# Optimization experiments

Hardware: AMD Instinct MI355X
Metric: run time of the kernel (lower is better)

Reference implementation:

```python
import jax, jax.numpy as jnp
import numpy as np

BS, GS, E, KMAX = 128, 2000, 128, 4
CLIP = 10.0
NEG = -1e30


def _gru(x, hprev, Wih, Whh, bih, bhh):
    # torch.nn.GRUCell math
    gi = x @ Wih.T + bih
    gh = hprev @ Whh.T + bhh
    ir, iz, i_n = jnp.split(gi, 3, axis=-1)
    hr, hz, h_n = jnp.split(gh, 3, axis=-1)
    r = jax.nn.sigmoid(ir + hr)
    z = jax.nn.sigmoid(iz + hz)
    n = jnp.tanh(i_n + r * h_n)
    return (1.0 - z) * n + z * hprev


def setup_inputs() -> dict:
    key = jax.random.key(0)
    it = iter(jax.random.split(key, 40))
    s = 1.0 / float(np.sqrt(E))
    u = lambda shape: jax.random.uniform(next(it), shape, jnp.float32, -s, s)
    inp = {
        "h": jax.random.normal(next(it), (BS, GS, E), jnp.float32),
        "rec": jax.random.randint(next(it), (BS, GS), 0, GS, dtype=jnp.int32),
        "context2": jax.random.normal(next(it), (BS, 9), jnp.float32),
        "visited_time": jax.random.randint(next(it), (BS, GS), 0, GS, dtype=jnp.int32),
        "last_action": jax.random.randint(next(it), (BS, 1), 0, GS, dtype=jnp.int32),
        "fixed_action": jax.random.randint(next(it), (BS, KMAX), 0, GS, dtype=jnp.int32),
    }
    for n in ["W_K1", "W_K2", "W_K3", "W_K4", "W_Q1", "W_Q2", "W_Q3", "W_Q4", "W_init"]:
        inp[n] = u((E, E))
    for n in ["b_init", "V1", "V2", "init_query"]:
        inp[n] = u((E,))
    for r in ["rnn1", "rnn2"]:
        inp[r + "_Wih"] = u((3 * E, E))
        inp[r + "_Whh"] = u((3 * E, E))
        inp[r + "_bih"] = u((3 * E,))
        inp[r + "_bhh"] = u((3 * E,))
    return inp


def _forward(h, rec, visited_time, last_action, fixed_action,
             W_K1, W_K2, W_K3, W_K4, W_Q1, W_Q2, W_Q3, W_Q4, V1, V2,
             W_init, b_init, init_query,
             rnn1_Wih, rnn1_Whh, rnn1_bih, rnn1_bhh,
             rnn2_Wih, rnn2_Whh, rnn2_bih, rnn2_bhh):
    bs, gs, e = h.shape
    cols = jnp.arange(gs)[None, :]          # [1, gs]
    rows = jnp.arange(bs)
    # K projections of h are loop-invariant: hoist them (same math as in-loop recompute)
    K1h = jnp.einsum('bge,fe->bgf', h, W_K1)
    K2h = jnp.einsum('bge,fe->bgf', h, W_K2)
    K3h = jnp.einsum('bge,fe->bgf', h, W_K3)
    K4h = jnp.einsum('bge,fe->bgf', h, W_K4)
    q1 = q2 = h.mean(1) @ W_init.T + b_init
    input_q1 = input_q2 = jnp.broadcast_to(init_query, (bs, e))
    mask = jnp.zeros((bs, gs), bool)
    stopped = jnp.ones((bs,), bool)
    nol = jnp.full((bs, 1), -1, jnp.int32)   # next_of_last_action
    ai = jnp.zeros((bs, KMAX), jnp.int32)    # action_index
    kl = jnp.zeros((bs, KMAX + 1), jnp.int32)
    kr = jnp.zeros((bs, KMAX), jnp.int32)
    ll = jnp.zeros((bs,), h.dtype)
    vtt = None
    for i in range(KMAX):
        q1 = _gru(input_q1, q1, rnn1_Wih, rnn1_Whh, rnn1_bih, rnn1_bhh)
        q2 = _gru(input_q2, q2, rnn2_Wih, rnn2_Whh, rnn2_bih, rnn2_bhh)
        s1 = (V1 * jnp.tanh(K1h + (q1 @ W_Q1.T)[:, None, :] + K3h * (q1 @ W_Q3.T)[:, None, :])).sum(-1)
        s2 = (V2 * jnp.tanh(K2h + (q2 @ W_Q2.T)[:, None, :] + K4h * (q2 @ W_Q4.T)[:, None, :])).sum(-1)
        logits = jnp.tanh(s1 + s2) * CLIP
        logits = jnp.where(mask, NEG, logits)
        if i == 0:
            logits = jnp.where(cols == last_action, NEG, logits)
        action = fixed_action[:, i:i + 1]
        if i > 0:
            action = jnp.where(stopped[:, None], ai[:, 0:1], action)
        logp = jax.nn.log_softmax(logits, axis=-1)
        loss_now = jnp.take_along_axis(logp, action, 1)[:, 0]
        ll = ll + (loss_now if i == 0 else jnp.where(stopped, 0.0, loss_now))
        nna = jnp.take_along_axis(rec, action, 1)  # next_of_new_action [bs,1]
        ai = ai.at[:, i].set(action[:, 0])
        kl = kl.at[:, i].set(jnp.where(stopped, action[:, 0], kl[:, i]))
        kr = kr.at[:, (i - 1) % KMAX].set(jnp.where(stopped, kr[:, (i - 1) % KMAX], action[:, 0]))
        kl = kl.at[:, i + 1].set(nna[:, 0])
        input_q1 = h[rows, action[:, 0]]
        input_q2 = jnp.where(stopped[:, None], input_q1, h[rows, nol[:, 0] % gs])
        eq = (action == nol)[:, 0]
        stopped = eq if i == 0 else (stopped | eq)
        kl = kl.at[:, i].set(jnp.where(stopped, kl[:, (i - 1) % (KMAX + 1)], kl[:, i]))
        kr = kr.at[:, i].set(jnp.where(stopped, kr[:, (i - 1) % KMAX], kr[:, i]))
        if i == 0:
            vtt = (visited_time - jnp.take_along_axis(visited_time, action, 1)) % gs
        vtt_a = jnp.take_along_axis(vtt, action, 1)
        mask = vtt <= vtt_a
        if i == 0:
            mask = mask | (vtt > gs - 2)
        mask = jnp.where(stopped[:, None] & (cols == action), False, mask)
        allow = (~stopped) & (nna[:, 0] == ai[:, 0])
        mask = jnp.where(allow[:, None] & (cols == ai[:, 0:1]), False, mask)
        nol = jnp.where(stopped[:, None], jnp.int32(-1), nna)
    kr = kr.at[:, KMAX - 1].set(jnp.where(~stopped, kl[:, KMAX], kr[:, KMAX - 1]))
    action_all = jnp.concatenate([ai, kl[:, :KMAX], kr], axis=-1)  # [bs, 3*KMAX]
    return action_all, ll


def reference(h, rec, context2, visited_time, last_action, fixed_action,
              W_K1, W_K2, W_K3, W_K4, W_Q1, W_Q2, W_Q3, W_Q4,
              V1, V2, W_init, b_init, init_query,
              rnn1_Wih, rnn1_Whh, rnn1_bih, rnn1_bhh,
              rnn2_Wih, rnn2_Whh, rnn2_bih, rnn2_bhh):
    # context2 unused: with_explore_stat_feature=False path (learned V1/V2)
    return _forward(h, rec, visited_time, last_action, fixed_action,
                    W_K1, W_K2, W_K3, W_K4, W_Q1, W_Q2, W_Q3, W_Q4, V1, V2,
                    W_init, b_init, init_query,
                    rnn1_Wih, rnn1_Whh, rnn1_bih, rnn1_bhh,
                    rnn2_Wih, rnn2_Whh, rnn2_bih, rnn2_bhh)
```

## Files before the change

### kernel.cpp

```cpp
#include <hip/hip_runtime.h>
#include <math.h>

#define BS 128
#define GS 2000
#define E  128
#define KMAXI 4
#define CLIPV 10.0f
#define NEGV  -1.0e30f

typedef __bf16 bf16_t;
typedef __bf16 bf16x8 __attribute__((ext_vector_type(8)));
typedef float fx4 __attribute__((ext_vector_type(4)));
typedef float fx2 __attribute__((ext_vector_type(2)));

__device__ __forceinline__ float fast_sigmoid(float x){ return 1.0f/(1.0f+__expf(-x)); }
__device__ __forceinline__ float fast_tanhf(float x){
    float e = __expf(2.0f*x);
    return 1.0f - 2.0f/(e + 1.0f);
}
__device__ __forceinline__ float pade_tanh(float x){
    float t = __builtin_amdgcn_fmed3f(x, -3.0f, 3.0f);
    float r = t*t;
    float num = t*(27.0f + r);
    float den = fmaf(9.0f, r, 27.0f);
    return num * __builtin_amdgcn_rcpf(den);
}
__device__ __forceinline__ fx2 tanh2_poly(fx2 x){
    fx2 t;
    t.x = __builtin_amdgcn_fmed3f(x.x, -3.0f, 3.0f);
    t.y = __builtin_amdgcn_fmed3f(x.y, -3.0f, 3.0f);
    fx2 r = t*t;
    fx2 q = r*(-0.0015650f) + 0.03172875f;
    q = q*r + (-0.23082094f);
    q = q*r + 0.979947f;
    return t*q;
}
__device__ __forceinline__ int pymod_s(int a){ return a < 0 ? a + GS : a; }

__device__ __forceinline__ void load_lds16(const bf16_t* g, bf16_t* l){
    __builtin_amdgcn_global_load_lds(
        (const __attribute__((address_space(1))) void*)g,
        (__attribute__((address_space(3))) void*)l, 16, 0, 0);
}

#define SC_STRIDE 64

__global__ __launch_bounds__(256) void k_hmean(
    const float* __restrict__ h, float* __restrict__ hpart,
    const int* __restrict__ rec, const int* __restrict__ vtime,
    const int* __restrict__ last_action, const int* __restrict__ fixed_action,
    int* __restrict__ sc, float* __restrict__ out)
{
    int b = blockIdx.x, p = blockIdx.y, tid = threadIdx.x;
    if (p == 16){
        if (b != 0) return;
        int t = tid;
        if (t >= BS) return;
        int stopped = 1, nol = -1;
        int ai[4]={0,0,0,0}, kl[5]={0,0,0,0,0}, kr[4]={0,0,0,0};
        int a0 = 0;
        int* scb = sc + t*SC_STRIDE;
        for (int it=0; it<KMAXI; ++it){
            int action = (it==0) ? fixed_action[t*KMAXI]
                                 : (stopped ? ai[0] : fixed_action[t*KMAXI+it]);
            int old_stopped = stopped;
            if (it==0) a0 = action;
            int vta = (it==0) ? 0 : pymod_s(vtime[(size_t)t*GS+action] - vtime[(size_t)t*GS+a0]);
            int nna = rec[(size_t)t*GS+action];
            int eq  = (action == nol) ? 1 : 0;
            int new_stopped = (it==0) ? eq : (stopped | eq);
            int ai0 = (it==0) ? action : ai[0];
            int allow = (!new_stopped) && (nna == ai0);

            ai[it] = action;
            if (old_stopped)  kl[it] = action;
            if (!old_stopped) kr[(it+3)&3] = action;
            kl[it+1] = nna;
            if (new_stopped) kl[it] = kl[(it+4)%5];
            if (new_stopped) kr[it] = kr[(it+3)&3];

            int row1 = action;
            int i2 = pymod_s(nol);
            int row2 = old_stopped ? row1 : i2;

            int* s_it = scb + 8 + it*8;
            s_it[0]=action; s_it[1]=old_stopped; s_it[2]=new_stopped;
            s_it[3]=allow;  s_it[4]=vta; s_it[5]=row1; s_it[6]=row2;

            nol = new_stopped ? -1 : nna;
            stopped = new_stopped;
        }
        scb[0] = a0;
        if (!stopped) kr[3] = kl[4];
        for (int j=0;j<4;++j) out[t*12+j]   = (float)ai[j];
        for (int j=0;j<4;++j) out[t*12+4+j] = (float)kl[j];
        for (int j=0;j<4;++j) out[t*12+8+j] = (float)kr[j];
        return;
    }
    int e4 = (tid & 31) * 4;
    int gsub = tid >> 5;
    float4 acc = {0.f,0.f,0.f,0.f};
    int g0 = p*125, g1 = g0+125;
    for (int g = g0 + gsub; g < g1; g += 8){
        float4 v = *(const float4*)(h + ((size_t)b*GS + g)*E + e4);
        acc.x += v.x; acc.y += v.y; acc.z += v.z; acc.w += v.w;
    }
    __shared__ float ps[8][E];
    *(float4*)(&ps[gsub][e4]) = acc;
    __syncthreads();
    if (tid < E){
        float s = 0.f;
        #pragma unroll
        for (int j=0;j<8;++j) s += ps[j][tid];
        hpart[(b*16+p)*E + tid] = s;
    }
}

__device__ __forceinline__ float dot32(const float* a, const float* __restrict__ w){
    const float4* a4=(const float4*)a; const float4* w4=(const float4*)w;
    float s=0.f;
    #pragma unroll 8
    for (int i=0;i<32;++i){ float4 x=a4[i], y=w4[i]; s += x.x*y.x + x.y*y.y + x.z*y.z + x.w*y.w; }
    return s;
}

__global__ __launch_bounds__(384) void k_gru4(
    const float* __restrict__ hpart, const float* __restrict__ W_init,
    const float* __restrict__ b_init, const float* __restrict__ init_query,
    const float* __restrict__ h, const int* __restrict__ sc,
    const float* __restrict__ Wih1, const float* __restrict__ Whh1,
    const float* __restrict__ bih1, const float* __restrict__ bhh1,
    const float* __restrict__ Wih2, const float* __restrict__ Whh2,
    const float* __restrict__ bih2, const float* __restrict__ bhh2,
    const float* __restrict__ WQ1, const float* __restrict__ WQ2,
    const float* __restrict__ WQ3, const float* __restrict__ WQ4,
    float* __restrict__ add_buf, float* __restrict__ mul_buf)
{
    int b = blockIdx.x, rnn = blockIdx.y, t = threadIdx.x;
    const float* Wih = rnn ? Wih2 : Wih1;
    const float* Whh = rnn ? Whh2 : Whh1;
    const float* bih = rnn ? bih2 : bih1;
    const float* bhh = rnn ? bhh2 : bhh1;
    const float* WQa = rnn ? WQ2 : WQ1;
    const float* WQm = rnn ? WQ4 : WQ3;

    __shared__ float xv[E], hv[E];
    __shared__ float gi_s[3*E], gh_s[3*E];

    if (t < E){
        float s = 0.f;
        for (int p=0;p<16;++p) s += hpart[(b*16+p)*E + t];
        xv[t] = s * (1.0f/(float)GS);
    }
    __syncthreads();
    if (t < E) hv[t] = b_init[t] + dot32(xv, W_init + (size_t)t*E);
    __syncthreads();
    if (t < E) xv[t] = init_query[t];
    __syncthreads();

    for (int s=0; s<KMAXI; ++s){
        if (s>0){
            if (t < E){
                int row = sc[b*SC_STRIDE + 8 + (s-1)*8 + (rnn==0 ? 5 : 6)];
                xv[t] = h[((size_t)b*GS + row)*E + t];
            }
            __syncthreads();
        }
        {
            float gi = bih[t] + dot32(xv, Wih + (size_t)t*E);
            float gh = bhh[t] + dot32(hv, Whh + (size_t)t*E);
            gi_s[t] = gi; gh_s[t] = gh;
        }
        __syncthreads();
        if (t < E){
            float r = fast_sigmoid(gi_s[t]     + gh_s[t]);
            float z = fast_sigmoid(gi_s[t+E]   + gh_s[t+E]);
            float n = fast_tanhf  (gi_s[t+2*E] + r*gh_s[t+2*E]);
            hv[t] = (1.f-z)*n + z*hv[t];
        }
        __syncthreads();
        if (t < 2*E){
            int r = t & (E-1);
            const float* W = (t < E) ? WQa : WQm;
            float v = dot32(hv, W + (size_t)r*E);
            int slot = s*2 + rnn;
            if (t < E) add_buf[(size_t)slot*BS*E + b*E + r] = v;
            else       mul_buf[(size_t)slot*BS*E + b*E + r] = v;
        }
        __syncthreads();
    }
}

__global__ __launch_bounds__(256) void k_mbuild(
    const float* __restrict__ WK1, const float* __restrict__ WK2,
    const float* __restrict__ WK3, const float* __restrict__ WK4,
    const float* __restrict__ mul_buf, bf16_t* __restrict__ Mb)
{
    int b = blockIdx.x, slot = blockIdx.y, tid = threadIdx.x;
    int arm = slot & 1;
    const float* WKa = arm ? WK2 : WK1;
    const float* WKm = arm ? WK4 : WK3;
    const float* mul = mul_buf + (size_t)slot*BS*E + b*E;
    __shared__ float mv[E];
    if (tid < E) mv[tid] = mul[tid];
    __syncthreads();
    bf16x8* outp = (bf16x8*)(Mb + ((size_t)slot*BS + b)*E*E);
    #pragma unroll
    for (int j=0;j<8;++j){
        int u = j*256 + tid;
        int f = u >> 4, e8 = u & 15;
        int e0 = e8*8;
        float mf = mv[f];
        float4 a0 = *(const float4*)(WKa + (size_t)f*E + e0);
        float4 a1 = *(const float4*)(WKa + (size_t)f*E + e0 + 4);
        float4 m0 = *(const float4*)(WKm + (size_t)f*E + e0);
        float4 m1 = *(const float4*)(WKm + (size_t)f*E + e0 + 4);
        bf16x8 o;
        o[0]=(bf16_t)(a0.x + m0.x*mf);
        o[1]=(bf16_t)(a0.y + m0.y*mf);
        o[2]=(bf16_t)(a0.z + m0.z*mf);
        o[3]=(bf16_t)(a0.w + m0.w*mf);
        o[4]=(bf16_t)(a1.x + m1.x*mf);
        o[5]=(bf16_t)(a1.y + m1.y*mf);
        o[6]=(bf16_t)(a1.z + m1.z*mf);
        o[7]=(bf16_t)(a1.w + m1.w*mf);
        outp[f*16 + (e8 ^ (f&7))] = o;
    }
}

__global__ __launch_bounds__(256,2) void k_scores(
    const float* __restrict__ hf, const bf16_t* __restrict__ Mb,
    const float* __restrict__ add_buf,
    const float* __restrict__ V1, const float* __restrict__ V2,
    const int* __restrict__ vtime, const int* __restrict__ last_action,
    const int* __restrict__ sc,
    float* __restrict__ part, float* __restrict__ act_val)
{
    __shared__ bf16_t sM[2][E*E];
    __shared__ float redm[16], reds[16];
    __shared__ float bmxs;
    int b = blockIdx.x, yc = blockIdx.y, tid = threadIdx.x;
    int wave = tid >> 6, lane = tid & 63;
    int qd = lane >> 4, cl = lane & 15;
    int gbase = yc*128 + wave*32;

    {
        const bf16_t* G0 = Mb + (size_t)b*E*E;
        #pragma unroll
        for (int j=0;j<8;++j){
            int c = wave*512 + j*64 + lane;
            load_lds16(G0 + (size_t)c*8, &sM[0][0] + (size_t)c*8);
        }
    }

    const int* scb = sc + b*SC_STRIDE;
    int a0s = scb[0];
    int la  = last_action[b];
    int vt0 = vtime[(size_t)b*GS + a0s];

    float vv_r[2][8];
    #pragma unroll
    for (int tf=0; tf<8; ++tf){
        vv_r[0][tf] = V1[tf*16+cl];
        vv_r[1][tf] = V2[tf*16+cl];
    }

    bf16x8 afr[2][4];
    #pragma unroll
    for (int set=0; set<2; ++set){
        int grow = gbase + set*16 + cl;
        if (grow >= GS) grow = GS-1;
        const float* hrow = hf + ((size_t)b*GS + grow)*E;
        #pragma unroll
        for (int s=0;s<4;++s){
            const float* p = hrow + s*32 + qd*8;
            float4 u0 = *(const float4*)(p);
            float4 u1 = *(const float4*)(p+4);
            bf16x8 a;
            a[0]=(bf16_t)u0.x; a[1]=(bf16_t)u0.y; a[2]=(bf16_t)u0.z; a[3]=(bf16_t)u0.w;
            a[4]=(bf16_t)u1.x; a[5]=(bf16_t)u1.y; a[6]=(bf16_t)u1.z; a[7]=(bf16_t)u1.w;
            afr[set][s]=a;
        }
    }
    __syncthreads();

    for (int it=0; it<KMAXI; ++it){
        fx2 s00={0.f,0.f}, s01={0.f,0.f}, s10={0.f,0.f}, s11={0.f,0.f};
        #pragma unroll
        for (int arm=0; arm<2; ++arm){
            int slot = it*2 + arm;
            int cur = slot & 1;
            if (slot < 7){
                const bf16_t* Gn = Mb + ((size_t)(slot+1)*BS + b)*E*E;
                #pragma unroll
                for (int j=0;j<8;++j){
                    int c = wave*512 + j*64 + lane;
                    load_lds16(Gn + (size_t)c*8, &sM[cur^1][0] + (size_t)c*8);
                }
            }
            const float* addv = add_buf + (size_t)slot*BS*E + b*E;
            float av_r[8];
            #pragma unroll
            for (int tf=0; tf<8; ++tf) av_r[tf] = addv[tf*16+cl];

            const bf16_t* sMc = &sM[cur][0];
            #pragma unroll
            for (int tf=0; tf<8; ++tf){
                int f = tf*16 + cl;
                bf16x8 b1[4];
                #pragma unroll
                for (int s=0;s<4;++s){
                    int e8 = s*4 + qd;
                    b1[s] = *(const bf16x8*)(sMc + ((size_t)(f*16 + (e8 ^ (f&7))))*8);
                }
                float av = av_r[tf];
                fx4 a0 = {av,av,av,av};
                fx4 a1 = {av,av,av,av};
                #pragma unroll
                for (int s=0;s<4;++s){
                    a0 = __builtin_amdgcn_mfma_f32_16x16x32_bf16(afr[0][s], b1[s], a0, 0,0,0);
                    a1 = __builtin_amdgcn_mfma_f32_16x16x32_bf16(afr[1][s], b1[s], a1, 0,0,0);
                }
                fx2 vv2 = {vv_r[arm][tf], vv_r[arm][tf]};
                s00 += vv2 * tanh2_poly((fx2){a0[0], a0[1]});
                s01 += vv2 * tanh2_poly((fx2){a0[2], a0[3]});
                s10 += vv2 * tanh2_poly((fx2){a1[0], a1[1]});
                s11 += vv2 * tanh2_poly((fx2){a1[2], a1[3]});
            }
            __syncthreads();
        }

        float vfin[2][4];
        #pragma unroll
        for (int set=0;set<2;++set){
            fx2 pa = set ? s10 : s00;
            fx2 pb = set ? s11 : s01;
            float v[4] = {pa.x, pa.y, pb.x, pb.y};
            #pragma unroll
            for (int r=0;r<4;++r){
                float s = v[r];
                s += __shfl_xor(s, 1); s += __shfl_xor(s, 2);
                s += __shfl_xor(s, 4); s += __shfl_xor(s, 8);
                vfin[set][r] = s;
            }
        }

        int act = scb[8 + it*8 + 0];
        int ap=0, nsp=0, alp=0, vtp=0;
        if (it>0){
            const int* s_p = scb + 8 + (it-1)*8;
            ap = s_p[0]; nsp = s_p[2]; alp = s_p[3]; vtp = s_p[4];
        }
        float x[8];
        float lm = NEGV;
        if (cl==0){
            #pragma unroll
            for (int set=0;set<2;++set){
                #pragma unroll
                for (int r=0;r<4;++r){
                    int idx = set*4 + r;
                    int g = gbase + set*16 + qd*4 + r;
                    float o = CLIPV*pade_tanh(vfin[set][r]);
                    int valid = (g < GS);
                    int gi = valid ? g : (GS-1);
                    int msk;
                    if (it==0){
                        msk = (g==la);
                    } else {
                        int d = vtime[(size_t)b*GS + gi] - vt0;
                        if (d < 0) d += GS;
                        msk = (d <= vtp) ? 1 : 0;
                        if (it==1 && d > GS-2) msk = 1;
                        if (nsp && g==ap)      msk = 0;
                        if (alp && g==a0s)     msk = 0;
                    }
                    float xx = (valid && !msk) ? o : NEGV;
                    if (valid && g==act) act_val[(size_t)it*BS + b] = xx;
                    x[idx] = xx;
                    lm = fmaxf(lm, xx);
                }
            }
            redm[wave*4+qd] = lm;
        }
        __syncthreads();
        if (tid==0){
            float m = redm[0];
            #pragma unroll
            for (int i=1;i<16;++i) m = fmaxf(m, redm[i]);
            bmxs = m;
        }
        __syncthreads();
        float bm = bmxs;
        if (cl==0){
            float ls = 0.f;
            #pragma unroll
            for (int i=0;i<8;++i) ls += __expf(x[i]-bm);
            reds[wave*4+qd] = ls;
        }
        __syncthreads();
        if (tid==0){
            float ss = 0.f;
            #pragma unroll
            for (int i=0;i<16;++i) ss += reds[i];
            fx2 pr = {bm, ss};
            *(fx2*)(part + (((size_t)it*BS + b)*16 + yc)*2) = pr;
        }
    }
}

__global__ __launch_bounds__(128) void k_final(
    const float* __restrict__ part, const float* __restrict__ act_val,
    const int* __restrict__ sc, float* __restrict__ out)
{
    int b = threadIdx.x;
    if (b >= BS) return;
    const int* scb = sc + b*SC_STRIDE;
    float ll = 0.f;
    for (int it=0; it<KMAXI; ++it){
        const fx2* pp = (const fx2*)(part + (((size_t)it*BS + b)*16)*2);
        float M = NEGV;
        #pragma unroll
        for (int i=0;i<16;++i) M = fmaxf(M, pp[i].x);
        float S = 0.f;
        #pragma unroll
        for (int i=0;i<16;++i) S += pp[i].y * __expf(pp[i].x - M);
        float lse = M + __logf(S);
        float av = act_val[(size_t)it*BS + b];
        int olds = scb[8 + it*8 + 1];
        if (it==0 || !olds) ll += av - lse;
    }
    out[BS*12 + b] = ll;
}

extern "C" void kernel_launch(void* const* d_in, const int* in_sizes, int n_in,
                              void* d_out, int out_size, void* d_ws, size_t ws_size,
                              hipStream_t stream)
{
    const float* h            = (const float*)d_in[0];
    const int*   rec          = (const int*)  d_in[1];
    const int*   vtime        = (const int*)  d_in[3];
    const int*   last_action  = (const int*)  d_in[4];
    const int*   fixed_action = (const int*)  d_in[5];
    const float* WK1=(const float*)d_in[6],  *WK2=(const float*)d_in[7];
    const float* WK3=(const float*)d_in[8],  *WK4=(const float*)d_in[9];
    const float* WQ1=(const float*)d_in[10], *WQ2=(const float*)d_in[11];
    const float* WQ3=(const float*)d_in[12], *WQ4=(const float*)d_in[13];
    const float* W_init=(const float*)d_in[14];
    const float* b_init=(const float*)d_in[15];
    const float* V1=(const float*)d_in[16], *V2=(const float*)d_in[17];
    const float* init_query=(const float*)d_in[18];
    const float* Wih1=(const float*)d_in[19], *Whh1=(const float*)d_in[20];
    const float* bih1=(const float*)d_in[21], *bhh1=(const float*)d_in[22];
    const float* Wih2=(const float*)d_in[23], *Whh2=(const float*)d_in[24];
    const float* bih2=(const float*)d_in[25], *bhh2=(const float*)d_in[26];
    float* out = (float*)d_out;

    char* ws = (char*)d_ws;
    size_t off = 0;
    auto alloc = [&](size_t bytes)->char*{
        char* p = ws + off; off += (bytes + 255) & ~(size_t)255; return p;
    };
    bf16_t* Mb     = (bf16_t*)alloc((size_t)8*BS*E*E*sizeof(bf16_t));
    float*  add_buf= (float*) alloc((size_t)8*BS*E*sizeof(float));
    float*  mul_buf= (float*) alloc((size_t)8*BS*E*sizeof(float));
    float*  hpart  = (float*) alloc((size_t)BS*16*E*sizeof(float));
    int*    sc     = (int*)   alloc((size_t)BS*SC_STRIDE*sizeof(int));
    float*  part   = (float*) alloc((size_t)KMAXI*BS*16*2*sizeof(float));
    float*  actv   = (float*) alloc((size_t)KMAXI*BS*sizeof(float));
    (void)in_sizes; (void)n_in; (void)out_size; (void)ws_size;

    hipLaunchKernelGGL(k_hmean, dim3(BS,17), dim3(256), 0, stream,
                       h, hpart, rec, vtime, last_action, fixed_action, sc, out);
    hipLaunchKernelGGL(k_gru4, dim3(BS,2), dim3(384), 0, stream,
                       hpart, W_init, b_init, init_query, h, sc,
                       Wih1,Whh1,bih1,bhh1, Wih2,Whh2,bih2,bhh2,
                       WQ1,WQ2,WQ3,WQ4, add_buf, mul_buf);
    hipLaunchKernelGGL(k_mbuild, dim3(BS,8), dim3(256), 0, stream,
                       WK1,WK2,WK3,WK4, mul_buf, Mb);
    hipLaunchKernelGGL(k_scores, dim3(BS,16), dim3(256), 0, stream,
                       h, Mb, add_buf, V1, V2, vtime, last_action, sc, part, actv);
    hipLaunchKernelGGL(k_final, dim3(1), dim3(128), 0, stream,
                       part, actv, sc, out);
}
```

Before: 460.5 us.

## Single-buffer M tile in LDS and move block softmax reduction to final kernel

```diff
diff --git a/kernel.cpp b/kernel.cpp
--- a/kernel.cpp
+++ b/kernel.cpp
@@ -236,22 +236,11 @@
     const int* __restrict__ sc,
     float* __restrict__ part, float* __restrict__ act_val)
 {
-    __shared__ bf16_t sM[2][E*E];
-    __shared__ float redm[16], reds[16];
-    __shared__ float bmxs;
+    __shared__ bf16_t sM[E*E];
     int b = blockIdx.x, yc = blockIdx.y, tid = threadIdx.x;
     int wave = tid >> 6, lane = tid & 63;
     int qd = lane >> 4, cl = lane & 15;
     int gbase = yc*128 + wave*32;
-
-    {
-        const bf16_t* G0 = Mb + (size_t)b*E*E;
-        #pragma unroll
-        for (int j=0;j<8;++j){
-            int c = wave*512 + j*64 + lane;
-            load_lds16(G0 + (size_t)c*8, &sM[0][0] + (size_t)c*8);
-        }
-    }
 
     const int* scb = sc + b*SC_STRIDE;
     int a0s = scb[0];
@@ -282,28 +271,27 @@
             afr[set][s]=a;
         }
     }
-    __syncthreads();
 
     for (int it=0; it<KMAXI; ++it){
         fx2 s00={0.f,0.f}, s01={0.f,0.f}, s10={0.f,0.f}, s11={0.f,0.f};
         #pragma unroll
         for (int arm=0; arm<2; ++arm){
             int slot = it*2 + arm;
-            int cur = slot & 1;
-            if (slot < 7){
-                const bf16_t* Gn = Mb + ((size_t)(slot+1)*BS + b)*E*E;
-                #pragma unroll
-                for (int j=0;j<8;++j){
-                    int c = wave*512 + j*64 + lane;
-                    load_lds16(Gn + (size_t)c*8, &sM[cur^1][0] + (size_t)c*8);
-                }
+            const bf16_t* Gm = Mb + ((size_t)slot*BS + b)*E*E;
+            const float* addv = add_buf + (size_t)slot*BS*E + b*E;
+
+            float av_r[8];
+            #pragma unroll
+            for (int tf=0; tf<8; ++tf) av_r[tf] = addv[tf*16+cl];
+
+            __syncthreads();
+            #pragma unroll
+            for (int j=0;j<8;++j){
+                int c = wave*512 + j*64 + lane;
+                load_lds16(Gm + (size_t)c*8, sM + (size_t)c*8);
             }
-            const float* addv = add_buf + (size_t)slot*BS*E + b*E;
-            float av_r[8];
-            #pragma unroll
-            for (int tf=0; tf<8; ++tf) av_r[tf] = addv[tf*16+cl];
-
-            const bf16_t* sMc = &sM[cur][0];
+            __syncthreads();
+
             #pragma unroll
             for (int tf=0; tf<8; ++tf){
                 int f = tf*16 + cl;
@@ -311,7 +299,7 @@
                 #pragma unroll
                 for (int s=0;s<4;++s){
                     int e8 = s*4 + qd;
-                    b1[s] = *(const bf16x8*)(sMc + ((size_t)(f*16 + (e8 ^ (f&7))))*8);
+                    b1[s] = *(const bf16x8*)(sM + ((size_t)(f*16 + (e8 ^ (f&7))))*8);
                 }
                 float av = av_r[tf];
                 fx4 a0 = {av,av,av,av};
@@ -327,7 +315,6 @@
                 s10 += vv2 * tanh2_poly((fx2){a1[0], a1[1]});
                 s11 += vv2 * tanh2_poly((fx2){a1[2], a1[3]});
             }
-            __syncthreads();
         }
 
         float vfin[2][4];
@@ -351,9 +338,9 @@
             const int* s_p = scb + 8 + (it-1)*8;
             ap = s_p[0]; nsp = s_p[2]; alp = s_p[3]; vtp = s_p[4];
         }
-        float x[8];
-        float lm = NEGV;
         if (cl==0){
+            float x[8];
+            float lm = NEGV;
             #pragma unroll
             for (int set=0;set<2;++set){
                 #pragma unroll
@@ -380,56 +367,46 @@
                     lm = fmaxf(lm, xx);
                 }
             }
-            redm[wave*4+qd] = lm;
-        }
-        __syncthreads();
-        if (tid==0){
-            float m = redm[0];
-            #pragma unroll
-            for (int i=1;i<16;++i) m = fmaxf(m, redm[i]);
-            bmxs = m;
-        }
-        __syncthreads();
-        float bm = bmxs;
-        if (cl==0){
             float ls = 0.f;
             #pragma unroll
-            for (int i=0;i<8;++i) ls += __expf(x[i]-bm);
-            reds[wave*4+qd] = ls;
-        }
-        __syncthreads();
-        if (tid==0){
-            float ss = 0.f;
-            #pragma unroll
-            for (int i=0;i<16;++i) ss += reds[i];
-            fx2 pr = {bm, ss};
-            *(fx2*)(part + (((size_t)it*BS + b)*16 + yc)*2) = pr;
-        }
-    }
-}
-
-__global__ __launch_bounds__(128) void k_final(
+            for (int i=0;i<8;++i) ls += __expf(x[i]-lm);
+            int pi = yc*16 + wave*4 + qd;
+            fx2 pr = {lm, ls};
+            *(fx2*)(part + (((size_t)it*BS + b)*256 + pi)*2) = pr;
+        }
+    }
+}
+
+__global__ __launch_bounds__(512) void k_final(
     const float* __restrict__ part, const float* __restrict__ act_val,
     const int* __restrict__ sc, float* __restrict__ out)
 {
-    int b = threadIdx.x;
-    if (b >= BS) return;
-    const int* scb = sc + b*SC_STRIDE;
-    float ll = 0.f;
-    for (int it=0; it<KMAXI; ++it){
-        const fx2* pp = (const fx2*)(part + (((size_t)it*BS + b)*16)*2);
+    __shared__ float lses[KMAXI][BS];
+    int t = threadIdx.x;
+    int it = t >> 7, b = t & 127;
+    {
+        const fx2* pp = (const fx2*)part + ((size_t)it*BS + b)*256;
         float M = NEGV;
+        #pragma unroll 8
+        for (int i=0;i<256;++i) M = fmaxf(M, pp[i].x);
+        float S = 0.f;
+        #pragma unroll 8
+        for (int i=0;i<256;++i){ fx2 p = pp[i]; S += p.y * __expf(p.x - M); }
+        lses[it][b] = M + __logf(S);
+    }
+    __syncthreads();
+    if (t < BS){
+        int b2 = t;
+        const int* scb = sc + b2*SC_STRIDE;
+        float ll = 0.f;
         #pragma unroll
-        for (int i=0;i<16;++i) M = fmaxf(M, pp[i].x);
-        float S = 0.f;
-        #pragma unroll
-        for (int i=0;i<16;++i) S += pp[i].y * __expf(pp[i].x - M);
-        float lse = M + __logf(S);
-        float av = act_val[(size_t)it*BS + b];
-        int olds = scb[8 + it*8 + 1];
-        if (it==0 || !olds) ll += av - lse;
-    }
-    out[BS*12 + b] = ll;
+        for (int i2=0; i2<KMAXI; ++i2){
+            int olds = scb[8 + i2*8 + 1];
+            float loss = act_val[(size_t)i2*BS + b2] - lses[i2][b2];
+            if (i2==0 || !olds) ll += loss;
+        }
+        out[BS*12 + b2] = ll;
+    }
 }
 
 extern "C" void kernel_launch(void* const* d_in, const int* in_sizes, int n_in,
@@ -465,7 +442,7 @@
     float*  mul_buf= (float*) alloc((size_t)8*BS*E*sizeof(float));
     float*  hpart  = (float*) alloc((size_t)BS*16*E*sizeof(float));
     int*    sc     = (int*)   alloc((size_t)BS*SC_STRIDE*sizeof(int));
-    float*  part   = (float*) alloc((size_t)KMAXI*BS*16*2*sizeof(float));
+    float*  part   = (float*) alloc((size_t)KMAXI*BS*256*2*sizeof(float));
     float*  actv   = (float*) alloc((size_t)KMAXI*BS*sizeof(float));
     (void)in_sizes; (void)n_in; (void)out_size; (void)ws_size;
 
@@ -479,6 +456,6 @@
                        WK1,WK2,WK3,WK4, mul_buf, Mb);
     hipLaunchKernelGGL(k_scores, dim3(BS,16), dim3(256), 0, stream,
                        h, Mb, add_buf, V1, V2, vtime, last_action, sc, part, actv);
-    hipLaunchKernelGGL(k_final, dim3(1), dim3(128), 0, stream,
+    hipLaunchKernelGGL(k_final, dim3(1), dim3(512), 0, stream,
                        part, actv, sc, out);
 }
```

New measurement: 506.1 us. +9.9%, slower.
